# Kernel optimization log

Hardware: AMD Instinct MI355X
Metric: run time of the kernel (lower is better)

The kernel has to match this reference:

```python
import jax, jax.numpy as jnp
import numpy as np

NUM_HEADS = 12


def _rope(t, cos, sin):
    # t: (B, H, M, D); cos/sin: (M, D//2) applied to interleaved pairs
    B, H, M, D = t.shape
    t2 = t.reshape(B, H, M, D // 2, 2)
    t0, t1 = t2[..., 0], t2[..., 1]
    c = cos[None, None]  # (1,1,M,D//2)
    s = sin[None, None]
    r0 = t0 * c - t1 * s
    r1 = t0 * s + t1 * c
    return jnp.stack([r0, r1], axis=-1).reshape(B, H, M, D)


def setup_inputs() -> dict:
    key = jax.random.key(0)
    ks = jax.random.split(key, 7)
    B, N, C = 16, 577, 768
    Hd = C // NUM_HEADS
    x = jax.random.normal(ks[0], (B, N, C), dtype=jnp.float32)
    # rotary angles for N-1 non-CLS tokens
    theta = jax.random.uniform(ks[1], (N - 1, Hd // 2), dtype=jnp.float32) * 6.28318
    cos = jnp.cos(theta)
    sin = jnp.sin(theta)
    w_qkv = jax.random.normal(ks[2], (C, 3 * C), dtype=jnp.float32) * 0.02
    b_qkv = jax.random.normal(ks[3], (3 * C,), dtype=jnp.float32) * 0.02
    w_proj = jax.random.normal(ks[4], (C, C), dtype=jnp.float32) * 0.02
    b_proj = jax.random.normal(ks[5], (C,), dtype=jnp.float32) * 0.02
    return {"x": x, "cos": cos, "sin": sin, "w_qkv": w_qkv, "b_qkv": b_qkv,
            "w_proj": w_proj, "b_proj": b_proj}


def reference(x, cos, sin, w_qkv, b_qkv, w_proj, b_proj):
    B, N, C = x.shape
    H = NUM_HEADS
    D = C // H
    scale = D ** -0.5
    qkv = x @ w_qkv + b_qkv                       # (B, N, 3C)
    qkv = qkv.reshape(B, N, 3, H, D).transpose(2, 0, 3, 1, 4)  # (3, B, H, N, D)
    q, k, v = qkv[0], qkv[1], qkv[2]
    # RoPE applied to all tokens except the CLS token (index 0)
    q = jnp.concatenate([q[:, :, :1], _rope(q[:, :, 1:], cos, sin)], axis=2)
    k = jnp.concatenate([k[:, :, :1], _rope(k[:, :, 1:], cos, sin)], axis=2)
    attn = jax.nn.softmax(jnp.einsum('bhnd,bhmd->bhnm', q, k) * scale, axis=-1)
    out = jnp.einsum('bhnm,bhmd->bhnd', attn, v)  # (B, H, N, D)
    out = out.transpose(0, 2, 1, 3).reshape(B, N, C)
    return out @ w_proj + b_proj
```

## Files before the change

kernel.cpp:

```cpp
#include <hip/hip_runtime.h>
#include <stdint.h>

typedef unsigned short u16;
typedef __attribute__((ext_vector_type(8))) short bf16x8;
typedef __attribute__((ext_vector_type(4))) float f32x4;

#define MFMA16(a, b, c) __builtin_amdgcn_mfma_f32_16x16x32_bf16((a), (b), (c), 0, 0, 0)

__device__ __forceinline__ float b2f(u16 u) {
    union { unsigned int i; float f; } v; v.i = ((unsigned int)u) << 16; return v.f;
}
__device__ __forceinline__ u16 f2b(float f) {
    union { float f; unsigned int i; } v; v.f = f;
    unsigned int r = v.i + 0x7fffu + ((v.i >> 16) & 1u);
    return (u16)(r >> 16);
}
__device__ __forceinline__ float exp2_fast(float x) {
    float r; __asm__("v_exp_f32 %0, %1" : "=v"(r) : "v"(x)); return r;
}

typedef __attribute__((address_space(1))) void gvoid;
typedef __attribute__((address_space(3))) void lvoid;
__device__ __forceinline__ void gld16(const void* g, void* l) {
    __builtin_amdgcn_global_load_lds((gvoid*)(void*)g, (lvoid*)l, 16, 0, 0);
}

__device__ __forceinline__ void tile_from_bid(int bid, int nTM, int nTN,
                                              int& rt, int& ct) {
    const int PW = 8;
    const int full = nTM / PW;
    const int per = PW * nTN;
    int p = bid / per;
    int pw = PW;
    int rem = bid - p * per;
    if (p >= full) { p = full; rem = bid - full * per; pw = nTM - full * PW; }
    const int c = rem / pw;
    const int r = rem - c * pw;
    rt = p * PW + r;
    ct = c;
}

__global__ __launch_bounds__(256) void f32_to_bf16(const float* __restrict__ in,
                                                   u16* __restrict__ out, int n) {
    const int i = (blockIdx.x * 256 + threadIdx.x) * 4;
    if (i + 3 < n) {
        const float4 v = *(const float4*)(in + i);
        ushort4 o;
        o.x = f2b(v.x); o.y = f2b(v.y); o.z = f2b(v.z); o.w = f2b(v.w);
        *(ushort4*)(out + i) = o;
    }
}

__global__ __launch_bounds__(256) void transpose_w(const float* __restrict__ wqkv,
                                                   const float* __restrict__ wproj,
                                                   u16* __restrict__ outQ,
                                                   u16* __restrict__ outP) {
    __shared__ float tile[32][33];
    int bx = blockIdx.x;
    const float* in; u16* out; int C;
    if (bx < 72) { in = wqkv; out = outQ; C = 2304; }
    else         { bx -= 72; in = wproj; out = outP; C = 768; }
    const int R = 768;
    const int t = threadIdx.x;
    const int r = t >> 3, c4 = (t & 7) * 4;
    const int ir = blockIdx.y * 32 + r, ic = bx * 32 + c4;
    const float4 v = *(const float4*)(in + (size_t)ir * C + ic);
    tile[r][c4 + 0] = v.x; tile[r][c4 + 1] = v.y;
    tile[r][c4 + 2] = v.z; tile[r][c4 + 3] = v.w;
    __syncthreads();
    const int orow = bx * 32 + r, ocol = blockIdx.y * 32 + c4;
    ushort4 o;
    o.x = f2b(tile[c4 + 0][r]); o.y = f2b(tile[c4 + 1][r]);
    o.z = f2b(tile[c4 + 2][r]); o.w = f2b(tile[c4 + 3][r]);
    *(ushort4*)(out + (size_t)orow * R + ocol) = o;
}

template <int EPI>
__global__ __launch_bounds__(512) void gemm_bt(const u16* __restrict__ A,
                                               const u16* __restrict__ Bt,
                                               const float* __restrict__ bias,
                                               void* __restrict__ Cv,
                                               const float* __restrict__ cosp,
                                               const float* __restrict__ sinp,
                                               u16* __restrict__ VtG,
                                               int M, int N, int K) {
    __shared__ __align__(16) u16 As0[128 * 64];
    __shared__ __align__(16) u16 As1[128 * 64];
    __shared__ __align__(16) u16 Bs0[128 * 64];
    __shared__ __align__(16) u16 Bs1[128 * 64];

    const int t = threadIdx.x;
    const int lane = t & 63;
    const int wave = t >> 6;
    const int l15 = lane & 15, quad = lane >> 4;
    const int wm = wave >> 2;
    const int wn = wave & 3;

    int rt, ct;
    tile_from_bid(blockIdx.y * gridDim.x + blockIdx.x, gridDim.x, gridDim.y, rt, ct);
    const int row0 = rt * 128;
    const int col0 = ct * 128;

    const f32x4 fz = {0.f, 0.f, 0.f, 0.f};
    f32x4 acc[4][2];
#pragma unroll
    for (int i = 0; i < 4; ++i)
#pragma unroll
        for (int j = 0; j < 2; ++j) acc[i][j] = fz;

    const u16* Ap[2];
    const u16* Bp[2];
    int off[2];
#pragma unroll
    for (int n = 0; n < 2; ++n) {
        const int g = t + n * 512;
        const int row = g >> 3;
        const int slot = (g & 7) ^ (row & 7);
        int ar = row0 + row; if (ar > M - 1) ar = M - 1;
        Ap[n] = A + (size_t)ar * K + slot * 8;
        Bp[n] = Bt + (size_t)(col0 + row) * K + slot * 8;
        off[n] = g * 8;
    }

#define STAGE(kt_, Ad, Bd) do {                                            \
        const int kb_ = (kt_) << 6;                                        \
        gld16(Ap[0] + kb_, (Ad) + off[0]);                                 \
        gld16(Ap[1] + kb_, (Ad) + off[1]);                                 \
        gld16(Bp[0] + kb_, (Bd) + off[0]);                                 \
        gld16(Bp[1] + kb_, (Bd) + off[1]);                                 \
    } while (0)

#define COMPUTE(Asb, Bsb) do {                                             \
        _Pragma("unroll")                                                  \
        for (int kk = 0; kk < 2; ++kk) {                                   \
            const int swk = ((kk * 4 + quad) ^ (l15 & 7)) * 8;             \
            bf16x8 af[4], bfr[2];                                          \
            _Pragma("unroll")                                              \
            for (int mi = 0; mi < 4; ++mi)                                 \
                af[mi] = *(const bf16x8*)((Asb) +                          \
                    ((wm * 4 + mi) * 16 + l15) * 64 + swk);                \
            _Pragma("unroll")                                              \
            for (int ni = 0; ni < 2; ++ni)                                 \
                bfr[ni] = *(const bf16x8*)((Bsb) +                         \
                    ((wn * 2 + ni) * 16 + l15) * 64 + swk);                \
            _Pragma("unroll")                                              \
            for (int mi = 0; mi < 4; ++mi)                                 \
                _Pragma("unroll")                                          \
                for (int ni = 0; ni < 2; ++ni)                             \
                    acc[mi][ni] = MFMA16(bfr[ni], af[mi], acc[mi][ni]);    \
        }                                                                  \
    } while (0)

    const int nKT = K >> 6;
    STAGE(0, As0, Bs0);
    __syncthreads();

    for (int kt = 0; kt < nKT; kt += 2) {
        if (kt + 1 < nKT) STAGE(kt + 1, As1, Bs1);
        COMPUTE(As0, Bs0);
        __syncthreads();
        if (kt + 2 < nKT) STAGE(kt + 2, As0, Bs0);
        COMPUTE(As1, Bs1);
        __syncthreads();
    }
#undef STAGE
#undef COMPUTE

    if (EPI == 2) {
        if (col0 >= 1536) {
#pragma unroll
            for (int mi = 0; mi < 4; ++mi) {
                const int row = row0 + wm * 64 + mi * 16 + l15;
                if (row < M) {
                    const int bb = row / 577, n = row - bb * 577;
                    u16* vdst = VtG + (size_t)bb * 491520 + n;
#pragma unroll
                    for (int ni = 0; ni < 2; ++ni) {
                        const int colb = col0 + wn * 32 + ni * 16 + quad * 4;
                        const float4 bv = *(const float4*)(bias + colb);
#pragma unroll
                        for (int r = 0; r < 4; ++r) {
                            const int cv = colb + r - 1536;
                            vdst[(size_t)(cv >> 6) * 40960 + (cv & 63) * 640] =
                                f2b(acc[mi][ni][r] + ((const float*)&bv)[r]);
                        }
                    }
                }
            }
        } else {
#pragma unroll
            for (int mi = 0; mi < 4; ++mi) {
                const int row = row0 + wm * 64 + mi * 16 + l15;
                if (row < M) {
                    const int bb = row / 577, n = row - bb * 577;
                    const bool hr = (n >= 1);
                    const float* cb = cosp + (size_t)(hr ? (n - 1) : 0) * 32;
                    const float* sb = sinp + (size_t)(hr ? (n - 1) : 0) * 32;
                    u16* outp = (u16*)Cv + (size_t)row * 1536;
#pragma unroll
                    for (int ni = 0; ni < 2; ++ni) {
                        const int colb = col0 + wn * 32 + ni * 16 + quad * 4;
                        const float4 bv = *(const float4*)(bias + colb);
                        const int pi = (colb & 63) >> 1;
                        float2 c = *(const float2*)(cb + pi);
                        float2 s = *(const float2*)(sb + pi);
                        if (!hr) { c.x = 1.f; c.y = 1.f; s.x = 0.f; s.y = 0.f; }
                        const float v0 = acc[mi][ni][0] + bv.x;
                        const float v1 = acc[mi][ni][1] + bv.y;
                        const float v2 = acc[mi][ni][2] + bv.z;
                        const float v3 = acc[mi][ni][3] + bv.w;
                        ushort4 o;
                        o.x = f2b(v0 * c.x - v1 * s.x);
                        o.y = f2b(v0 * s.x + v1 * c.x);
                        o.z = f2b(v2 * c.y - v3 * s.y);
                        o.w = f2b(v2 * s.y + v3 * c.y);
                        *(ushort4*)(outp + colb) = o;
                    }
                }
            }
        }
    } else {
#pragma unroll
        for (int ni = 0; ni < 2; ++ni) {
            const int colb = col0 + wn * 32 + ni * 16 + quad * 4;
            const float4 bv = *(const float4*)(bias + colb);
#pragma unroll
            for (int mi = 0; mi < 4; ++mi) {
                const int row = row0 + wm * 64 + mi * 16 + l15;
                if (row < M) {
                    float4 o;
                    o.x = acc[mi][ni][0] + bv.x; o.y = acc[mi][ni][1] + bv.y;
                    o.z = acc[mi][ni][2] + bv.z; o.w = acc[mi][ni][3] + bv.w;
                    *(float4*)((float*)Cv + (size_t)row * N + colb) = o;
                }
            }
        }
    }
}

#define PSTR 72
#define CEXP 0.18033688011112042f

__global__ __launch_bounds__(256) void attn2(const u16* __restrict__ qkv,
                                             const u16* __restrict__ VtG,
                                             u16* __restrict__ aout) {
    __shared__ __align__(16) u16 Ks0[64 * 64];
    __shared__ __align__(16) u16 Ks1[64 * 64];
    __shared__ __align__(16) u16 Vs0[64 * 64];
    __shared__ __align__(16) u16 Vs1[64 * 64];
    __shared__ __align__(16) u16 Pb[4 * 16 * PSTR];

    const int t = threadIdx.x;
    const int lane = t & 63, wave = t >> 6;
    const int l15 = lane & 15, quad = lane >> 4;

    const int bid = blockIdx.x;
    const int swz = (bid & 7) * 240 + (bid >> 3);
    const int bh = swz / 10, qt = swz - bh * 10;
    const int b = bh / 12, h = bh - b * 12;
    const u16* baseQ = qkv + (size_t)b * 577 * 1536 + h * 64;
    const u16* baseK = baseQ + 768;
    const u16* vbase = VtG + (size_t)bh * 64 * 640;

    const int mq = qt * 64 + wave * 16 + l15;
    const int nq = mq < 577 ? mq : 576;
    bf16x8 aq[2];
    aq[0] = *(const bf16x8*)(baseQ + (size_t)nq * 1536 + quad * 8);
    aq[1] = *(const bf16x8*)(baseQ + (size_t)nq * 1536 + 32 + quad * 8);

    const int g0 = t, g1 = t + 256;
    const int r0 = g0 >> 3, r1 = g1 >> 3;
    const int s0 = (g0 & 7) ^ (r0 & 7), s1 = (g1 & 7) ^ (r1 & 7);
    const int o0 = g0 * 8, o1 = g1 * 8;
    const u16* Kp0 = baseK + (size_t)r0 * 1536 + s0 * 8;
    const u16* Kp1 = baseK + (size_t)r1 * 1536 + s1 * 8;
    const u16* Vp0 = vbase + (size_t)r0 * 640 + s0 * 8;
    const u16* Vp1 = vbase + (size_t)r1 * 640 + s1 * 8;
    const u16* K9p0 = baseK + (size_t)576 * 1536 + s0 * 8;
    const u16* K9p1 = baseK + (size_t)576 * 1536 + s1 * 8;

    const int swk0 = (quad ^ (l15 & 7)) * 8;
    const int swk1 = ((4 + quad) ^ (l15 & 7)) * 8;

    u16* Pw = Pb + wave * 16 * PSTR;

    f32x4 oacc[4];
    const f32x4 fz = {0.f, 0.f, 0.f, 0.f};
#pragma unroll
    for (int i = 0; i < 4; ++i) oacc[i] = fz;
    float m4[4] = {-1e30f, -1e30f, -1e30f, -1e30f};
    float l4[4] = {0.f, 0.f, 0.f, 0.f};

#define ASTAGE(kt_, Kd, Vd) do {                                            \
        gld16(Kp0 + (size_t)(kt_) * 98304, (Kd) + o0);                      \
        gld16(Kp1 + (size_t)(kt_) * 98304, (Kd) + o1);                      \
        gld16(Vp0 + (kt_) * 64, (Vd) + o0);                                 \
        gld16(Vp1 + (kt_) * 64, (Vd) + o1);                                 \
    } while (0)

#define ASTAGE9(Kd, Vd) do {                                                \
        gld16(K9p0, (Kd) + o0);                                             \
        gld16(K9p1, (Kd) + o1);                                             \
        gld16(Vp0 + 576, (Vd) + o0);                                        \
        gld16(Vp1 + 576, (Vd) + o1);                                        \
    } while (0)

#define ATT_TILE(kt_, Kb, Vb, MASKED) do {                                  \
        f32x4 sacc[4];                                                      \
        _Pragma("unroll")                                                   \
        for (int nt = 0; nt < 4; ++nt) {                                    \
            sacc[nt] = fz;                                                  \
            const bf16x8 bk0 = *(const bf16x8*)((Kb) + (nt * 16 + l15) * 64 + swk0); \
            sacc[nt] = MFMA16(aq[0], bk0, sacc[nt]);                        \
            const bf16x8 bk1 = *(const bf16x8*)((Kb) + (nt * 16 + l15) * 64 + swk1); \
            sacc[nt] = MFMA16(aq[1], bk1, sacc[nt]);                        \
        }                                                                   \
        float sv[4][4];                                                     \
        _Pragma("unroll")                                                   \
        for (int nt = 0; nt < 4; ++nt)                                      \
            _Pragma("unroll")                                               \
            for (int r = 0; r < 4; ++r) {                                   \
                float s_ = sacc[nt][r];                                     \
                if (MASKED && ((kt_) * 64 + nt * 16 + l15 > 576)) s_ = -1e30f; \
                sv[nt][r] = s_;                                             \
            }                                                               \
        float mt[4];                                                        \
        _Pragma("unroll")                                                   \
        for (int r = 0; r < 4; ++r) {                                       \
            mt[r] = fmaxf(fmaxf(sv[0][r], sv[1][r]), fmaxf(sv[2][r], sv[3][r])); \
            _Pragma("unroll")                                               \
            for (int off = 1; off <= 8; off <<= 1)                          \
                mt[r] = fmaxf(mt[r], __shfl_xor(mt[r], off));               \
        }                                                                   \
        float alpha[4], nmc[4];                                             \
        _Pragma("unroll")                                                   \
        for (int r = 0; r < 4; ++r) {                                       \
            const float mnew = fmaxf(m4[r], mt[r]);                         \
            alpha[r] = exp2_fast((m4[r] - mnew) * CEXP);                    \
            m4[r] = mnew;                                                   \
            nmc[r] = -mnew * CEXP;                                          \
        }                                                                   \
        float lsum[4] = {0.f, 0.f, 0.f, 0.f};                               \
        _Pragma("unroll")                                                   \
        for (int nt = 0; nt < 4; ++nt)                                      \
            _Pragma("unroll")                                               \
            for (int r = 0; r < 4; ++r) {                                   \
                const float p = exp2_fast(__builtin_fmaf(sv[nt][r], CEXP, nmc[r])); \
                lsum[r] += p;                                               \
                Pw[(quad * 4 + r) * PSTR + nt * 16 + l15] = f2b(p);         \
            }                                                               \
        _Pragma("unroll")                                                   \
        for (int r = 0; r < 4; ++r) {                                       \
            _Pragma("unroll")                                               \
            for (int off = 1; off <= 8; off <<= 1)                          \
                lsum[r] += __shfl_xor(lsum[r], off);                        \
            l4[r] = l4[r] * alpha[r] + lsum[r];                             \
        }                                                                   \
        _Pragma("unroll")                                                   \
        for (int dt = 0; dt < 4; ++dt)                                      \
            _Pragma("unroll")                                               \
            for (int r = 0; r < 4; ++r) oacc[dt][r] *= alpha[r];            \
        __asm__ __volatile__("s_waitcnt lgkmcnt(0)" ::: "memory");          \
        _Pragma("unroll")                                                   \
        for (int kc = 0; kc < 2; ++kc) {                                    \
            const bf16x8 pf = *(const bf16x8*)(Pw + l15 * PSTR + kc * 32 + quad * 8); \
            const int swkv = kc ? swk1 : swk0;                              \
            _Pragma("unroll")                                               \
            for (int dt = 0; dt < 4; ++dt) {                                \
                const bf16x8 vf = *(const bf16x8*)((Vb) + (dt * 16 + l15) * 64 + swkv); \
                oacc[dt] = MFMA16(pf, vf, oacc[dt]);                        \
            }                                                               \
        }                                                                   \
    } while (0)

    ASTAGE(0, Ks0, Vs0);
    __syncthreads();

    for (int kt2 = 0; kt2 < 8; kt2 += 2) {
        ASTAGE(kt2 + 1, Ks1, Vs1);
        ATT_TILE(kt2, Ks0, Vs0, false);
        __syncthreads();
        ASTAGE(kt2 + 2, Ks0, Vs0);
        ATT_TILE(kt2 + 1, Ks1, Vs1, false);
        __syncthreads();
    }
    ASTAGE9(Ks1, Vs1);
    ATT_TILE(8, Ks0, Vs0, false);
    __syncthreads();
    ATT_TILE(9, Ks1, Vs1, true);

#undef ASTAGE
#undef ASTAGE9
#undef ATT_TILE

    float linv[4];
#pragma unroll
    for (int r = 0; r < 4; ++r) linv[r] = 1.f / l4[r];
#pragma unroll
    for (int r = 0; r < 4; ++r) {
        const int n = qt * 64 + wave * 16 + quad * 4 + r;
        if (n < 577) {
            u16* op = aout + ((size_t)b * 577 + n) * 768 + h * 64 + l15;
#pragma unroll
            for (int dt = 0; dt < 4; ++dt)
                op[dt * 16] = f2b(oacc[dt][r] * linv[r]);
        }
    }
}

extern "C" void kernel_launch(void* const* d_in, const int* in_sizes, int n_in,
                              void* d_out, int out_size, void* d_ws, size_t ws_size,
                              hipStream_t stream) {
    const float* x      = (const float*)d_in[0];
    const float* cosp   = (const float*)d_in[1];
    const float* sinp   = (const float*)d_in[2];
    const float* w_qkv  = (const float*)d_in[3];
    const float* b_qkv  = (const float*)d_in[4];
    const float* w_proj = (const float*)d_in[5];
    const float* b_proj = (const float*)d_in[6];
    float* out = (float*)d_out;

    char* ws = (char*)d_ws;
    u16* xb     = (u16*)(ws);
    u16* aout   = (u16*)(ws);
    u16* wqkvT  = (u16*)(ws + 14180352);
    u16* wprojT = (u16*)(ws + 17719296);
    u16* qkv    = (u16*)(ws + 18898944);
    u16* VtG    = (u16*)(ws + 47259648);

    f32_to_bf16<<<6924, 256, 0, stream>>>(x, xb, 7090176);
    transpose_w<<<dim3(96, 24), 256, 0, stream>>>(w_qkv, w_proj, wqkvT, wprojT);
    gemm_bt<2><<<dim3(73, 18), 512, 0, stream>>>(xb, wqkvT, b_qkv, qkv,
                                                 cosp, sinp, VtG, 9232, 2304, 768);
    attn2<<<dim3(1920), 256, 0, stream>>>(qkv, VtG, aout);
    gemm_bt<1><<<dim3(73, 6), 512, 0, stream>>>(aout, wprojT, b_proj, out,
                                                nullptr, nullptr, nullptr, 9232, 768, 768);
}
```

Measured before the change: 229.6 us.

## Transpose attention MFMA operands so each lane owns one query row

Swaps the A/B operands of the QK^T and PV MFMAs so the accumulator holds S^T and O^T. Each lane now owns a single query row, so the softmax max and sum need only two cross-lane shuffles instead of four per row times four rows. P is written to LDS as packed 4-element stores, and the output is written as 8-byte vector stores. The mask condition for the last tile is rewritten to match the new layout, and it relies on the fixed sequence length of 577.

New measurement: 218.0 us. 1.05x faster.

```diff
diff --git a/kernel.cpp b/kernel.cpp
--- a/kernel.cpp
+++ b/kernel.cpp
@@ -288,8 +288,8 @@
     const f32x4 fz = {0.f, 0.f, 0.f, 0.f};
 #pragma unroll
     for (int i = 0; i < 4; ++i) oacc[i] = fz;
-    float m4[4] = {-1e30f, -1e30f, -1e30f, -1e30f};
-    float l4[4] = {0.f, 0.f, 0.f, 0.f};
+    float m1 = -1e30f;
+    float l1 = 0.f;
 
 #define ASTAGE(kt_, Kd, Vd) do {                                            \
         gld16(Kp0 + (size_t)(kt_) * 98304, (Kd) + o0);                      \
@@ -311,55 +311,45 @@
         for (int nt = 0; nt < 4; ++nt) {                                    \
             sacc[nt] = fz;                                                  \
             const bf16x8 bk0 = *(const bf16x8*)((Kb) + (nt * 16 + l15) * 64 + swk0); \
-            sacc[nt] = MFMA16(aq[0], bk0, sacc[nt]);                        \
+            sacc[nt] = MFMA16(bk0, aq[0], sacc[nt]);                        \
             const bf16x8 bk1 = *(const bf16x8*)((Kb) + (nt * 16 + l15) * 64 + swk1); \
-            sacc[nt] = MFMA16(aq[1], bk1, sacc[nt]);                        \
+            sacc[nt] = MFMA16(bk1, aq[1], sacc[nt]);                        \
         }                                                                   \
-        float sv[4][4];                                                     \
+        if (MASKED) {                                                       \
+            _Pragma("unroll")                                               \
+            for (int nt = 0; nt < 4; ++nt)                                  \
+                _Pragma("unroll")                                           \
+                for (int r = 0; r < 4; ++r)                                 \
+                    if (nt * 16 + quad * 4 + r > 0) sacc[nt][r] = -1e30f;   \
+        }                                                                   \
+        float mA = fmaxf(fmaxf(sacc[0][0], sacc[0][1]), fmaxf(sacc[0][2], sacc[0][3])); \
+        float mB = fmaxf(fmaxf(sacc[1][0], sacc[1][1]), fmaxf(sacc[1][2], sacc[1][3])); \
+        float mC = fmaxf(fmaxf(sacc[2][0], sacc[2][1]), fmaxf(sacc[2][2], sacc[2][3])); \
+        float mD = fmaxf(fmaxf(sacc[3][0], sacc[3][1]), fmaxf(sacc[3][2], sacc[3][3])); \
+        float mt = fmaxf(fmaxf(mA, mB), fmaxf(mC, mD));                     \
+        mt = fmaxf(mt, __shfl_xor(mt, 16));                                 \
+        mt = fmaxf(mt, __shfl_xor(mt, 32));                                 \
+        const float mnew = fmaxf(m1, mt);                                   \
+        const float alpha = exp2_fast((m1 - mnew) * CEXP);                  \
+        m1 = mnew;                                                          \
+        const float nmc = -mnew * CEXP;                                     \
+        float lsum = 0.f;                                                   \
         _Pragma("unroll")                                                   \
-        for (int nt = 0; nt < 4; ++nt)                                      \
-            _Pragma("unroll")                                               \
-            for (int r = 0; r < 4; ++r) {                                   \
-                float s_ = sacc[nt][r];                                     \
-                if (MASKED && ((kt_) * 64 + nt * 16 + l15 > 576)) s_ = -1e30f; \
-                sv[nt][r] = s_;                                             \
-            }                                                               \
-        float mt[4];                                                        \
-        _Pragma("unroll")                                                   \
-        for (int r = 0; r < 4; ++r) {                                       \
-            mt[r] = fmaxf(fmaxf(sv[0][r], sv[1][r]), fmaxf(sv[2][r], sv[3][r])); \
-            _Pragma("unroll")                                               \
-            for (int off = 1; off <= 8; off <<= 1)                          \
-                mt[r] = fmaxf(mt[r], __shfl_xor(mt[r], off));               \
-        }                                                                   \
-        float alpha[4], nmc[4];                                             \
-        _Pragma("unroll")                                                   \
-        for (int r = 0; r < 4; ++r) {                                       \
-            const float mnew = fmaxf(m4[r], mt[r]);                         \
-            alpha[r] = exp2_fast((m4[r] - mnew) * CEXP);                    \
-            m4[r] = mnew;                                                   \
-            nmc[r] = -mnew * CEXP;                                          \
-        }                                                                   \
-        float lsum[4] = {0.f, 0.f, 0.f, 0.f};                               \
-        _Pragma("unroll")                                                   \
-        for (int nt = 0; nt < 4; ++nt)                                      \
-            _Pragma("unroll")                                               \
-            for (int r = 0; r < 4; ++r) {                                   \
-                const float p = exp2_fast(__builtin_fmaf(sv[nt][r], CEXP, nmc[r])); \
-                lsum[r] += p;                                               \
-                Pw[(quad * 4 + r) * PSTR + nt * 16 + l15] = f2b(p);         \
-            }                                                               \
-        _Pragma("unroll")                                                   \
-        for (int r = 0; r < 4; ++r) {                                       \
-            _Pragma("unroll")                                               \
-            for (int off = 1; off <= 8; off <<= 1)                          \
-                lsum[r] += __shfl_xor(lsum[r], off);                        \
-            l4[r] = l4[r] * alpha[r] + lsum[r];                             \
+        for (int nt = 0; nt < 4; ++nt) {                                    \
+            const float p0 = exp2_fast(__builtin_fmaf(sacc[nt][0], CEXP, nmc)); \
+            const float p1 = exp2_fast(__builtin_fmaf(sacc[nt][1], CEXP, nmc)); \
+            const float p2 = exp2_fast(__builtin_fmaf(sacc[nt][2], CEXP, nmc)); \
+            const float p3 = exp2_fast(__builtin_fmaf(sacc[nt][3], CEXP, nmc)); \
+            lsum += (p0 + p1) + (p2 + p3);                                  \
+            ushort4 pk;                                                     \
+            pk.x = f2b(p0); pk.y = f2b(p1); pk.z = f2b(p2); pk.w = f2b(p3); \
+            *(ushort4*)(Pw + l15 * PSTR + nt * 16 + quad * 4) = pk;         \
         }                                                                   \
         _Pragma("unroll")                                                   \
-        for (int dt = 0; dt < 4; ++dt)                                      \
-            _Pragma("unroll")                                               \
-            for (int r = 0; r < 4; ++r) oacc[dt][r] *= alpha[r];            \
+        for (int dt = 0; dt < 4; ++dt) {                                    \
+            oacc[dt][0] *= alpha; oacc[dt][1] *= alpha;                     \
+            oacc[dt][2] *= alpha; oacc[dt][3] *= alpha;                     \
+        }                                                                   \
         __asm__ __volatile__("s_waitcnt lgkmcnt(0)" ::: "memory");          \
         _Pragma("unroll")                                                   \
         for (int kc = 0; kc < 2; ++kc) {                                    \
@@ -368,9 +358,12 @@
             _Pragma("unroll")                                               \
             for (int dt = 0; dt < 4; ++dt) {                                \
                 const bf16x8 vf = *(const bf16x8*)((Vb) + (dt * 16 + l15) * 64 + swkv); \
-                oacc[dt] = MFMA16(pf, vf, oacc[dt]);                        \
+                oacc[dt] = MFMA16(vf, pf, oacc[dt]);                        \
             }                                                               \
         }                                                                   \
+        lsum += __shfl_xor(lsum, 16);                                       \
+        lsum += __shfl_xor(lsum, 32);                                       \
+        l1 = l1 * alpha + lsum;                                             \
     } while (0)
 
     ASTAGE(0, Ks0, Vs0);
@@ -393,17 +386,16 @@
 #undef ASTAGE9
 #undef ATT_TILE
 
-    float linv[4];
-#pragma unroll
-    for (int r = 0; r < 4; ++r) linv[r] = 1.f / l4[r];
-#pragma unroll
-    for (int r = 0; r < 4; ++r) {
-        const int n = qt * 64 + wave * 16 + quad * 4 + r;
-        if (n < 577) {
-            u16* op = aout + ((size_t)b * 577 + n) * 768 + h * 64 + l15;
-#pragma unroll
-            for (int dt = 0; dt < 4; ++dt)
-                op[dt * 16] = f2b(oacc[dt][r] * linv[r]);
+    const int n = qt * 64 + wave * 16 + l15;
+    if (n < 577) {
+        const float linv = 1.f / l1;
+        u16* op = aout + ((size_t)b * 577 + n) * 768 + h * 64 + quad * 4;
+#pragma unroll
+        for (int dt = 0; dt < 4; ++dt) {
+            ushort4 o;
+            o.x = f2b(oacc[dt][0] * linv); o.y = f2b(oacc[dt][1] * linv);
+            o.z = f2b(oacc[dt][2] * linv); o.w = f2b(oacc[dt][3] * linv);
+            *(ushort4*)(op + dt * 16) = o;
         }
     }
 }
```
